# Kernel optimization log

Hardware: AMD Instinct MI355X
Metric: run time of the kernel (lower is better)

Reference implementation:

```python
import jax, jax.numpy as jnp
import numpy as np

N = 100000
C_IN, C_OUT = 128, 64
BN_EPS = 1e-5
SLOPE = 0.01  # torch LeakyReLU default


def setup_inputs() -> dict:
    key = jax.random.key(0)
    ks = jax.random.split(key, 12)

    def w(k, K, cin, cout):
        return jax.random.normal(k, (K, cin, cout), jnp.float32) / np.sqrt(K * cin)

    x_feats = jax.random.normal(ks[0], (N, C_IN), jnp.float32)
    skip_feats = jax.random.normal(ks[1], (N, C_OUT), jnp.float32)
    W1 = w(ks[2], 27, C_IN, C_OUT)
    Wt = w(ks[3], 27, C_OUT, C_OUT)
    W2 = w(ks[4], 9, C_OUT, C_OUT)
    W3 = w(ks[5], 9, C_OUT, C_OUT)
    W4 = w(ks[6], 27, C_OUT, C_OUT)
    # bn[l] = (gamma, beta, running_mean, running_var) for BN layer l
    gamma = 1.0 + 0.01 * jax.random.normal(ks[7], (4, C_OUT), jnp.float32)
    beta = 0.01 * jax.random.normal(ks[8], (4, C_OUT), jnp.float32)
    mean = 0.1 * jax.random.normal(ks[9], (4, C_OUT), jnp.float32)
    var = jax.random.uniform(ks[10], (4, C_OUT), jnp.float32, 0.5, 1.5)
    bn = jnp.stack([gamma, beta, mean, var], axis=1)  # [4, 4, C_OUT]

    nk = jax.random.split(ks[11], 5)
    nbr1 = jax.random.randint(nk[0], (27, N), 0, N, jnp.int64)
    nbrt = jax.random.randint(nk[1], (27, N), 0, N, jnp.int64)
    nbr2 = jax.random.randint(nk[2], (9, N), 0, N, jnp.int64)
    nbr3 = jax.random.randint(nk[3], (9, N), 0, N, jnp.int64)
    nbr4 = jax.random.randint(nk[4], (27, N), 0, N, jnp.int64)
    return dict(x_feats=x_feats, skip_feats=skip_feats, W1=W1, Wt=Wt, W2=W2,
                W3=W3, W4=W4, bn=bn, nbr1=nbr1, nbrt=nbrt, nbr2=nbr2,
                nbr3=nbr3, nbr4=nbr4)


def sparse_conv(feats, W, nbr):
    """Gather-GEMM-accumulate sparse conv.

    feats: [N, Cin]; W: [K, Cin, Cout]; nbr: [K, N] neighbor index per tap.
    out[i] = sum_k feats[nbr[k, i]] @ W[k]
    """
    acc0 = jnp.zeros((feats.shape[0], W.shape[-1]), feats.dtype)

    def step(acc, wn):
        w_k, idx_k = wn
        return acc + feats[idx_k] @ w_k, None

    out, _ = jax.lax.scan(step, acc0, (W, nbr))
    return out


def bn_lrelu(x, p):
    gamma, beta, mean, var = p[0], p[1], p[2], p[3]
    y = (x - mean) * jax.lax.rsqrt(var + BN_EPS) * gamma + beta
    return jnp.where(y >= 0, y, SLOPE * y)


def reference(x_feats, skip_feats, W1, Wt, W2, W3, W4, bn,
              nbr1, nbrt, nbr2, nbr3, nbr4):
    # up_block: conv3x3x3 + BN + LeakyReLU, then transposed conv (no BN/act)
    h = bn_lrelu(sparse_conv(x_feats, W1, nbr1), bn[0])
    h = sparse_conv(h, Wt, nbrt)
    h = h + skip_feats  # out.feats += skip.feats
    # conv_x3: three conv blocks
    h = bn_lrelu(sparse_conv(h, W2, nbr2), bn[1])
    h = bn_lrelu(sparse_conv(h, W3, nbr3), bn[2])
    h = bn_lrelu(sparse_conv(h, W4, nbr4), bn[3])
    return h
```

## Files before the change

### kernel.cpp

```cpp
#include <hip/hip_runtime.h>
#include <stdint.h>


typedef __bf16 bf16x8 __attribute__((ext_vector_type(8)));
typedef float f32x16 __attribute__((ext_vector_type(16)));

__device__ __forceinline__ uint16_t f2bf(float f) {
    uint32_t u = __builtin_bit_cast(uint32_t, f);
    u = (u + 0x7fffu + ((u >> 16) & 1u)) >> 16;
    return (uint16_t)u;
}

__device__ __forceinline__ bf16x8 ldb8(const uint16_t* p) {
    return __builtin_bit_cast(bf16x8, *reinterpret_cast<const uint4*>(p));
}

__global__ void convert_x(const float* __restrict__ in, uint16_t* __restrict__ out, int n8) {
    int t = blockIdx.x * blockDim.x + threadIdx.x;
    if (t >= n8) return;
    const float4* p = reinterpret_cast<const float4*>(in) + 2 * (size_t)t;
    float4 f0 = p[0], f1 = p[1];
    uint32_t w0 = (uint32_t)f2bf(f0.x) | ((uint32_t)f2bf(f0.y) << 16);
    uint32_t w1 = (uint32_t)f2bf(f0.z) | ((uint32_t)f2bf(f0.w) << 16);
    uint32_t w2 = (uint32_t)f2bf(f1.x) | ((uint32_t)f2bf(f1.y) << 16);
    uint32_t w3 = (uint32_t)f2bf(f1.z) | ((uint32_t)f2bf(f1.w) << 16);
    uint4 v; v.x = w0; v.y = w1; v.z = w2; v.w = w3;
    *reinterpret_cast<uint4*>(out + 8 * (size_t)t) = v;
}

__global__ void pack_weights(const float* __restrict__ w1, const float* __restrict__ wt,
                             const float* __restrict__ w2, const float* __restrict__ w3,
                             const float* __restrict__ w4, const float* __restrict__ bn,
                             uint16_t* __restrict__ p1, uint16_t* __restrict__ pt,
                             uint16_t* __restrict__ p2, uint16_t* __restrict__ p3,
                             uint16_t* __restrict__ p4, float* __restrict__ bnps) {
    int w = blockIdx.y;
    int t = blockIdx.x * blockDim.x + threadIdx.x;
    if (w == 5) {
        if (t < 256) {
            int l = t >> 6, c = t & 63;
            float g = bn[(l * 4 + 0) * 64 + c];
            float b = bn[(l * 4 + 1) * 64 + c];
            float m = bn[(l * 4 + 2) * 64 + c];
            float v = bn[(l * 4 + 3) * 64 + c];
            float sc = g * rsqrtf(v + 1e-5f);
            bnps[(l * 2 + 0) * 64 + c] = sc;
            bnps[(l * 2 + 1) * 64 + c] = b - m * sc;
        }
        return;
    }
    const float* src; uint16_t* dst; int K, CIN;
    switch (w) {
        case 0:  src = w1; dst = p1; K = 27; CIN = 128; break;
        case 1:  src = wt; dst = pt; K = 27; CIN = 64;  break;
        case 2:  src = w2; dst = p2; K = 9;  CIN = 64;  break;
        case 3:  src = w3; dst = p3; K = 9;  CIN = 64;  break;
        default: src = w4; dst = p4; K = 27; CIN = 64;  break;
    }
    int S = CIN / 16;
    int F = K * S * 2 * 64;
    if (t >= F) return;
    int lane = t & 63;
    int r = t >> 6;
    int nt = r & 1; r >>= 1;
    int s = r % S;
    int k = r / S;
    int c = nt * 32 + (lane & 31);
    int cib = s * 16 + (lane >> 5) * 8;
    #pragma unroll
    for (int j = 0; j < 8; ++j)
        dst[(size_t)t * 8 + j] = f2bf(src[((size_t)k * CIN + cib + j) * 64 + c]);
}

template <int CIN, int MODE>
__global__ __launch_bounds__(64)
void conv_layer(const uint16_t* __restrict__ feats,
                const uint16_t* __restrict__ wf,
                const int* __restrict__ nbr,
                const int K, const int npts,
                const float* __restrict__ bnp,
                const float* __restrict__ skip,
                uint16_t* __restrict__ outb,
                float* __restrict__ outf) {
    constexpr int S = CIN / 16;
    const int lane = threadIdx.x;
    const int l31  = lane & 31;
    const int hi   = lane >> 5;
    const int base = blockIdx.x * 64;
    const int r0 = base + l31;
    const int r1 = r0 + 32;
    const int g0 = min(r0, npts - 1);
    const int g1 = min(r1, npts - 1);

    f32x16 acc00 = {0,0,0,0,0,0,0,0,0,0,0,0,0,0,0,0};
    f32x16 acc01 = {0,0,0,0,0,0,0,0,0,0,0,0,0,0,0,0};
    f32x16 acc10 = {0,0,0,0,0,0,0,0,0,0,0,0,0,0,0,0};
    f32x16 acc11 = {0,0,0,0,0,0,0,0,0,0,0,0,0,0,0,0};

    for (int k = 0; k < K; ++k) {
        const int i0 = nbr[(size_t)k * npts + g0];
        const int i1 = nbr[(size_t)k * npts + g1];
        const uint16_t* a0p = feats + (size_t)i0 * CIN + hi * 8;
        const uint16_t* a1p = feats + (size_t)i1 * CIN + hi * 8;
        const uint16_t* bp  = wf + (size_t)k * (S * 1024) + lane * 8;
        #pragma unroll
        for (int s = 0; s < S; ++s) {
            bf16x8 a0 = ldb8(a0p + s * 16);
            bf16x8 a1 = ldb8(a1p + s * 16);
            bf16x8 b0 = ldb8(bp + s * 1024);
            bf16x8 b1 = ldb8(bp + s * 1024 + 512);
            acc00 = __builtin_amdgcn_mfma_f32_32x32x16_bf16(a0, b0, acc00, 0, 0, 0);
            acc01 = __builtin_amdgcn_mfma_f32_32x32x16_bf16(a0, b1, acc01, 0, 0, 0);
            acc10 = __builtin_amdgcn_mfma_f32_32x32x16_bf16(a1, b0, acc10, 0, 0, 0);
            acc11 = __builtin_amdgcn_mfma_f32_32x32x16_bf16(a1, b1, acc11, 0, 0, 0);
        }
    }

    const int c0 = l31, c1 = 32 + l31;
    float sc0 = 0.f, sh0 = 0.f, sc1 = 0.f, sh1 = 0.f;
    if (MODE != 1) {
        sc0 = bnp[c0]; sh0 = bnp[64 + c0];
        sc1 = bnp[c1]; sh1 = bnp[64 + c1];
    }
    #pragma unroll
    for (int reg = 0; reg < 16; ++reg) {
        const int row = (reg & 3) + 8 * (reg >> 2) + 4 * hi;
        const int gr0 = base + row;
        const int gr1 = base + 32 + row;
        float v00 = acc00[reg], v01 = acc01[reg];
        float v10 = acc10[reg], v11 = acc11[reg];
        if (MODE != 1) {
            v00 = v00 * sc0 + sh0; v00 = v00 >= 0.f ? v00 : 0.01f * v00;
            v01 = v01 * sc1 + sh1; v01 = v01 >= 0.f ? v01 : 0.01f * v01;
            v10 = v10 * sc0 + sh0; v10 = v10 >= 0.f ? v10 : 0.01f * v10;
            v11 = v11 * sc1 + sh1; v11 = v11 >= 0.f ? v11 : 0.01f * v11;
        }
        if (gr0 < npts) {
            if (MODE == 1) { v00 += skip[(size_t)gr0 * 64 + c0]; v01 += skip[(size_t)gr0 * 64 + c1]; }
            if (MODE == 2) {
                outf[(size_t)gr0 * 64 + c0] = v00; outf[(size_t)gr0 * 64 + c1] = v01;
            } else {
                outb[(size_t)gr0 * 64 + c0] = f2bf(v00); outb[(size_t)gr0 * 64 + c1] = f2bf(v01);
            }
        }
        if (gr1 < npts) {
            if (MODE == 1) { v10 += skip[(size_t)gr1 * 64 + c0]; v11 += skip[(size_t)gr1 * 64 + c1]; }
            if (MODE == 2) {
                outf[(size_t)gr1 * 64 + c0] = v10; outf[(size_t)gr1 * 64 + c1] = v11;
            } else {
                outb[(size_t)gr1 * 64 + c0] = f2bf(v10); outb[(size_t)gr1 * 64 + c1] = f2bf(v11);
            }
        }
    }
}

extern "C" void kernel_launch(void* const* d_in, const int* in_sizes, int n_in,
                              void* d_out, int out_size, void* d_ws, size_t ws_size,
                              hipStream_t stream) {
    const int N = in_sizes[0] / 128;
    const float* x    = (const float*)d_in[0];
    const float* skip = (const float*)d_in[1];
    const float* W1   = (const float*)d_in[2];
    const float* Wt   = (const float*)d_in[3];
    const float* W2   = (const float*)d_in[4];
    const float* W3   = (const float*)d_in[5];
    const float* W4   = (const float*)d_in[6];
    const float* bn   = (const float*)d_in[7];
    const int* nbr1   = (const int*)d_in[8];
    const int* nbrt   = (const int*)d_in[9];
    const int* nbr2   = (const int*)d_in[10];
    const int* nbr3   = (const int*)d_in[11];
    const int* nbr4   = (const int*)d_in[12];

    uint8_t* ws = (uint8_t*)d_ws;
    size_t off = 0;
    auto carve = [&](size_t bytes) -> void* {
        void* p = ws + off;
        off += (bytes + 255) & ~(size_t)255;
        return p;
    };
    uint16_t* xb  = (uint16_t*)carve((size_t)N * 128 * 2);
    uint16_t* hA  = (uint16_t*)carve((size_t)N * 64 * 2);
    uint16_t* hB  = (uint16_t*)carve((size_t)N * 64 * 2);
    uint16_t* p1  = (uint16_t*)carve((size_t)27 * 128 * 64 * 2);
    uint16_t* pt  = (uint16_t*)carve((size_t)27 * 64 * 64 * 2);
    uint16_t* p2  = (uint16_t*)carve((size_t)9 * 64 * 64 * 2);
    uint16_t* p3  = (uint16_t*)carve((size_t)9 * 64 * 64 * 2);
    uint16_t* p4  = (uint16_t*)carve((size_t)27 * 64 * 64 * 2);
    float*    bnp = (float*)carve((size_t)4 * 2 * 64 * 4);

    const int n8 = N * 16;
    convert_x<<<(n8 + 255) / 256, 256, 0, stream>>>(x, xb, n8);
    pack_weights<<<dim3(108, 6), 256, 0, stream>>>(W1, Wt, W2, W3, W4, bn,
                                                   p1, pt, p2, p3, p4, bnp);

    const int grid = (N + 63) / 64;
    conv_layer<128, 0><<<grid, 64, 0, stream>>>(xb, p1, nbr1, 27, N, bnp + 0,   nullptr, hA, nullptr);
    conv_layer<64,  1><<<grid, 64, 0, stream>>>(hA, pt, nbrt, 27, N, nullptr,   skip,    hB, nullptr);
    conv_layer<64,  0><<<grid, 64, 0, stream>>>(hB, p2, nbr2, 9,  N, bnp + 128, nullptr, hA, nullptr);
    conv_layer<64,  0><<<grid, 64, 0, stream>>>(hA, p3, nbr3, 9,  N, bnp + 256, nullptr, hB, nullptr);
    conv_layer<64,  2><<<grid, 64, 0, stream>>>(hB, p4, nbr4, 27, N, bnp + 384, nullptr, nullptr, (float*)d_out);
}
```

Measured before the change: 537.1 us.

## Split kernel taps across two waves with LDS reduction and prefetched gathers

Each block now covers 32 points with two waves. Each wave handles half of the kernel taps, and the two partial accumulators are summed through shared memory. For CIN=64 layers the next tap's neighbor rows are prefetched into registers while the current tap's MFMAs run. Neighbor indices use nontemporal loads, and the epilogue writes vectorized, coalesced rows instead of scattered scalar stores. This is meant to raise parallelism and memory-level latency hiding in the gather. In exchange, each B-weight fragment now feeds only one 32-row tile rather than two, and the change adds an LDS round trip and a block barrier.

```diff
diff --git a/kernel.cpp b/kernel.cpp
--- a/kernel.cpp
+++ b/kernel.cpp
@@ -72,85 +72,134 @@
         dst[(size_t)t * 8 + j] = f2bf(src[((size_t)k * CIN + cib + j) * 64 + c]);
 }
 
-template <int CIN, int MODE>
-__global__ __launch_bounds__(64)
+template <int CIN, int K, int MODE>
+__global__ __launch_bounds__(128, 4)
 void conv_layer(const uint16_t* __restrict__ feats,
                 const uint16_t* __restrict__ wf,
                 const int* __restrict__ nbr,
-                const int K, const int npts,
+                const int npts,
                 const float* __restrict__ bnp,
                 const float* __restrict__ skip,
                 uint16_t* __restrict__ outb,
                 float* __restrict__ outf) {
     constexpr int S = CIN / 16;
-    const int lane = threadIdx.x;
+    constexpr int KH = K / 2;
+    constexpr bool PREF = (CIN == 64);
+    constexpr int RS = 68;
+    __shared__ float red[2 * 32 * RS];
+
+    const int tid  = threadIdx.x;
+    const int wave = tid >> 6;
+    const int lane = tid & 63;
     const int l31  = lane & 31;
     const int hi   = lane >> 5;
-    const int base = blockIdx.x * 64;
-    const int r0 = base + l31;
-    const int r1 = r0 + 32;
-    const int g0 = min(r0, npts - 1);
-    const int g1 = min(r1, npts - 1);
-
-    f32x16 acc00 = {0,0,0,0,0,0,0,0,0,0,0,0,0,0,0,0};
-    f32x16 acc01 = {0,0,0,0,0,0,0,0,0,0,0,0,0,0,0,0};
-    f32x16 acc10 = {0,0,0,0,0,0,0,0,0,0,0,0,0,0,0,0};
-    f32x16 acc11 = {0,0,0,0,0,0,0,0,0,0,0,0,0,0,0,0};
-
-    for (int k = 0; k < K; ++k) {
-        const int i0 = nbr[(size_t)k * npts + g0];
-        const int i1 = nbr[(size_t)k * npts + g1];
-        const uint16_t* a0p = feats + (size_t)i0 * CIN + hi * 8;
-        const uint16_t* a1p = feats + (size_t)i1 * CIN + hi * 8;
-        const uint16_t* bp  = wf + (size_t)k * (S * 1024) + lane * 8;
-        #pragma unroll
-        for (int s = 0; s < S; ++s) {
-            bf16x8 a0 = ldb8(a0p + s * 16);
-            bf16x8 a1 = ldb8(a1p + s * 16);
-            bf16x8 b0 = ldb8(bp + s * 1024);
-            bf16x8 b1 = ldb8(bp + s * 1024 + 512);
-            acc00 = __builtin_amdgcn_mfma_f32_32x32x16_bf16(a0, b0, acc00, 0, 0, 0);
-            acc01 = __builtin_amdgcn_mfma_f32_32x32x16_bf16(a0, b1, acc01, 0, 0, 0);
-            acc10 = __builtin_amdgcn_mfma_f32_32x32x16_bf16(a1, b0, acc10, 0, 0, 0);
-            acc11 = __builtin_amdgcn_mfma_f32_32x32x16_bf16(a1, b1, acc11, 0, 0, 0);
-        }
-    }
-
-    const int c0 = l31, c1 = 32 + l31;
-    float sc0 = 0.f, sh0 = 0.f, sc1 = 0.f, sh1 = 0.f;
-    if (MODE != 1) {
-        sc0 = bnp[c0]; sh0 = bnp[64 + c0];
-        sc1 = bnp[c1]; sh1 = bnp[64 + c1];
-    }
+    const int base = blockIdx.x * 32;
+    const int g0   = min(base + l31, npts - 1);
+
+    const int k0  = wave ? KH : 0;
+    const int cnt = wave ? (K - KH) : KH;
+
+    const int* nb = nbr + (size_t)k0 * npts + g0;
+    const uint16_t* wb = wf + (size_t)k0 * (S * 1024) + lane * 8;
+
+    f32x16 acc0 = {0,0,0,0,0,0,0,0,0,0,0,0,0,0,0,0};
+    f32x16 acc1 = {0,0,0,0,0,0,0,0,0,0,0,0,0,0,0,0};
+
+    int ic = __builtin_nontemporal_load(nb);
+    int i1 = (cnt > 1) ? __builtin_nontemporal_load(nb + (size_t)npts) : 0;
+
+    if constexpr (PREF) {
+        bf16x8 ac[S], an[S];
+        {
+            const uint16_t* ap = feats + (size_t)ic * CIN + hi * 8;
+            #pragma unroll
+            for (int s = 0; s < S; ++s) ac[s] = ldb8(ap + s * 16);
+        }
+        for (int kk = 0; kk < cnt; ++kk) {
+            const int i2 = (kk + 2 < cnt)
+                ? __builtin_nontemporal_load(nb + (size_t)(kk + 2) * npts) : 0;
+            if (kk + 1 < cnt) {
+                const uint16_t* ap = feats + (size_t)i1 * CIN + hi * 8;
+                #pragma unroll
+                for (int s = 0; s < S; ++s) an[s] = ldb8(ap + s * 16);
+            }
+            const uint16_t* bp = wb + (size_t)kk * (S * 1024);
+            #pragma unroll
+            for (int s = 0; s < S; ++s) {
+                bf16x8 b0 = ldb8(bp + s * 1024);
+                bf16x8 b1 = ldb8(bp + s * 1024 + 512);
+                acc0 = __builtin_amdgcn_mfma_f32_32x32x16_bf16(ac[s], b0, acc0, 0, 0, 0);
+                acc1 = __builtin_amdgcn_mfma_f32_32x32x16_bf16(ac[s], b1, acc1, 0, 0, 0);
+            }
+            if (kk + 1 < cnt) {
+                #pragma unroll
+                for (int s = 0; s < S; ++s) ac[s] = an[s];
+            }
+            i1 = i2;
+        }
+    } else {
+        for (int kk = 0; kk < cnt; ++kk) {
+            const int i2 = (kk + 2 < cnt)
+                ? __builtin_nontemporal_load(nb + (size_t)(kk + 2) * npts) : 0;
+            const uint16_t* ap = feats + (size_t)ic * CIN + hi * 8;
+            bf16x8 ac[S];
+            #pragma unroll
+            for (int s = 0; s < S; ++s) ac[s] = ldb8(ap + s * 16);
+            const uint16_t* bp = wb + (size_t)kk * (S * 1024);
+            #pragma unroll
+            for (int s = 0; s < S; ++s) {
+                bf16x8 b0 = ldb8(bp + s * 1024);
+                bf16x8 b1 = ldb8(bp + s * 1024 + 512);
+                acc0 = __builtin_amdgcn_mfma_f32_32x32x16_bf16(ac[s], b0, acc0, 0, 0, 0);
+                acc1 = __builtin_amdgcn_mfma_f32_32x32x16_bf16(ac[s], b1, acc1, 0, 0, 0);
+            }
+            ic = i1; i1 = i2;
+        }
+    }
+
     #pragma unroll
     for (int reg = 0; reg < 16; ++reg) {
         const int row = (reg & 3) + 8 * (reg >> 2) + 4 * hi;
-        const int gr0 = base + row;
-        const int gr1 = base + 32 + row;
-        float v00 = acc00[reg], v01 = acc01[reg];
-        float v10 = acc10[reg], v11 = acc11[reg];
-        if (MODE != 1) {
-            v00 = v00 * sc0 + sh0; v00 = v00 >= 0.f ? v00 : 0.01f * v00;
-            v01 = v01 * sc1 + sh1; v01 = v01 >= 0.f ? v01 : 0.01f * v01;
-            v10 = v10 * sc0 + sh0; v10 = v10 >= 0.f ? v10 : 0.01f * v10;
-            v11 = v11 * sc1 + sh1; v11 = v11 >= 0.f ? v11 : 0.01f * v11;
-        }
-        if (gr0 < npts) {
-            if (MODE == 1) { v00 += skip[(size_t)gr0 * 64 + c0]; v01 += skip[(size_t)gr0 * 64 + c1]; }
-            if (MODE == 2) {
-                outf[(size_t)gr0 * 64 + c0] = v00; outf[(size_t)gr0 * 64 + c1] = v01;
-            } else {
-                outb[(size_t)gr0 * 64 + c0] = f2bf(v00); outb[(size_t)gr0 * 64 + c1] = f2bf(v01);
-            }
-        }
-        if (gr1 < npts) {
-            if (MODE == 1) { v10 += skip[(size_t)gr1 * 64 + c0]; v11 += skip[(size_t)gr1 * 64 + c1]; }
-            if (MODE == 2) {
-                outf[(size_t)gr1 * 64 + c0] = v10; outf[(size_t)gr1 * 64 + c1] = v11;
-            } else {
-                outb[(size_t)gr1 * 64 + c0] = f2bf(v10); outb[(size_t)gr1 * 64 + c1] = f2bf(v11);
-            }
-        }
+        red[wave * (32 * RS) + row * RS + l31]      = acc0[reg];
+        red[wave * (32 * RS) + row * RS + 32 + l31] = acc1[reg];
+    }
+    __syncthreads();
+
+    const int er = tid >> 2;
+    const int ec = (tid & 3) * 16;
+    const int grow = base + er;
+    if (grow >= npts) return;
+
+    float v[16];
+    #pragma unroll
+    for (int j = 0; j < 16; ++j)
+        v[j] = red[er * RS + ec + j] + red[32 * RS + er * RS + ec + j];
+
+    if constexpr (MODE == 1) {
+        const float* sp = skip + (size_t)grow * 64 + ec;
+        #pragma unroll
+        for (int j = 0; j < 16; ++j) v[j] += sp[j];
+    } else {
+        #pragma unroll
+        for (int j = 0; j < 16; ++j) {
+            float y = v[j] * bnp[ec + j] + bnp[64 + ec + j];
+            v[j] = y >= 0.f ? y : 0.01f * y;
+        }
+    }
+
+    if constexpr (MODE == 2) {
+        float4* op = reinterpret_cast<float4*>(outf + (size_t)grow * 64 + ec);
+        #pragma unroll
+        for (int q = 0; q < 4; ++q)
+            op[q] = make_float4(v[4*q+0], v[4*q+1], v[4*q+2], v[4*q+3]);
+    } else {
+        uint32_t w[8];
+        #pragma unroll
+        for (int q = 0; q < 8; ++q)
+            w[q] = (uint32_t)f2bf(v[2*q]) | ((uint32_t)f2bf(v[2*q+1]) << 16);
+        uint4* op = reinterpret_cast<uint4*>(outb + (size_t)grow * 64 + ec);
+        op[0] = make_uint4(w[0], w[1], w[2], w[3]);
+        op[1] = make_uint4(w[4], w[5], w[6], w[7]);
     }
 }
 
@@ -194,10 +243,10 @@
     pack_weights<<<dim3(108, 6), 256, 0, stream>>>(W1, Wt, W2, W3, W4, bn,
                                                    p1, pt, p2, p3, p4, bnp);
 
-    const int grid = (N + 63) / 64;
-    conv_layer<128, 0><<<grid, 64, 0, stream>>>(xb, p1, nbr1, 27, N, bnp + 0,   nullptr, hA, nullptr);
-    conv_layer<64,  1><<<grid, 64, 0, stream>>>(hA, pt, nbrt, 27, N, nullptr,   skip,    hB, nullptr);
-    conv_layer<64,  0><<<grid, 64, 0, stream>>>(hB, p2, nbr2, 9,  N, bnp + 128, nullptr, hA, nullptr);
-    conv_layer<64,  0><<<grid, 64, 0, stream>>>(hA, p3, nbr3, 9,  N, bnp + 256, nullptr, hB, nullptr);
-    conv_layer<64,  2><<<grid, 64, 0, stream>>>(hB, p4, nbr4, 27, N, bnp + 384, nullptr, nullptr, (float*)d_out);
-}
+    const int grid = (N + 31) / 32;
+    conv_layer<128, 27, 0><<<grid, 128, 0, stream>>>(xb, p1, nbr1, N, bnp + 0,   nullptr, hA, nullptr);
+    conv_layer<64,  27, 1><<<grid, 128, 0, stream>>>(hA, pt, nbrt, N, nullptr,   skip,    hB, nullptr);
+    conv_layer<64,   9, 0><<<grid, 128, 0, stream>>>(hB, p2, nbr2, N, bnp + 128, nullptr, hA, nullptr);
+    conv_layer<64,   9, 0><<<grid, 128, 0, stream>>>(hA, p3, nbr3, N, bnp + 256, nullptr, hB, nullptr);
+    conv_layer<64,  27, 2><<<grid, 128, 0, stream>>>(hB, p4, nbr4, N, bnp + 384, nullptr, nullptr, (float*)d_out);
+}
```

Result: no change. 544.6 us (+1.4%).

## Stage gathered neighbor rows through swizzled LDS with register prefetch of next tap

Applied to the files above, without the earlier changes.

Each tap's gathered feature rows are now loaded with row-contiguous vector loads, with the index broadcast by shuffle. They are held in registers, then written to an XOR-swizzled shared-memory tile, and the MFMA operands are read back from that tile. The loads for tap k+1 and the neighbor index for tap k+2 are issued before the MFMAs of tap k run, so gather latency overlaps compute. K becomes a template parameter so the loops fully specialize. This costs extra registers for the staging buffer and an LDS round-trip, and relies on single-wave ordering because there is no barrier.

```diff
diff --git a/kernel.cpp b/kernel.cpp
--- a/kernel.cpp
+++ b/kernel.cpp
@@ -72,41 +72,73 @@
         dst[(size_t)t * 8 + j] = f2bf(src[((size_t)k * CIN + cib + j) * 64 + c]);
 }
 
-template <int CIN, int MODE>
+template <int CIN, int K, int MODE>
 __global__ __launch_bounds__(64)
 void conv_layer(const uint16_t* __restrict__ feats,
                 const uint16_t* __restrict__ wf,
                 const int* __restrict__ nbr,
-                const int K, const int npts,
+                const int npts,
                 const float* __restrict__ bnp,
                 const float* __restrict__ skip,
                 uint16_t* __restrict__ outb,
                 float* __restrict__ outf) {
-    constexpr int S = CIN / 16;
+    constexpr int S    = CIN / 16;
+    constexpr int CPR  = CIN / 8;
+    constexpr int RPI  = 64 / CPR;
+    constexpr int NSTG = CPR;
+    __shared__ uint4 sm4[64 * CPR];
+
     const int lane = threadIdx.x;
     const int l31  = lane & 31;
     const int hi   = lane >> 5;
+    const int xr   = l31 & 7;
     const int base = blockIdx.x * 64;
-    const int r0 = base + l31;
-    const int r1 = r0 + 32;
-    const int g0 = min(r0, npts - 1);
-    const int g1 = min(r1, npts - 1);
+    const int g    = min(base + lane, npts - 1);
+
+    const int sub = lane >> ((CPR == 16) ? 4 : 3);
+    const int t   = lane & (CPR - 1);
+
+    const uint16_t* sm = (const uint16_t*)sm4;
 
     f32x16 acc00 = {0,0,0,0,0,0,0,0,0,0,0,0,0,0,0,0};
     f32x16 acc01 = {0,0,0,0,0,0,0,0,0,0,0,0,0,0,0,0};
     f32x16 acc10 = {0,0,0,0,0,0,0,0,0,0,0,0,0,0,0,0};
     f32x16 acc11 = {0,0,0,0,0,0,0,0,0,0,0,0,0,0,0,0};
 
-    for (int k = 0; k < K; ++k) {
-        const int i0 = nbr[(size_t)k * npts + g0];
-        const int i1 = nbr[(size_t)k * npts + g1];
-        const uint16_t* a0p = feats + (size_t)i0 * CIN + hi * 8;
-        const uint16_t* a1p = feats + (size_t)i1 * CIN + hi * 8;
-        const uint16_t* bp  = wf + (size_t)k * (S * 1024) + lane * 8;
+    uint4 st[NSTG];
+
+    {
+        const int idx0 = nbr[g];
+        #pragma unroll
+        for (int it = 0; it < NSTG; ++it) {
+            const int row = it * RPI + sub;
+            const int src = __shfl(idx0, row);
+            st[it] = *reinterpret_cast<const uint4*>(feats + (size_t)src * CIN + t * 8);
+        }
+    }
+    int idxn = (K > 1) ? nbr[(size_t)npts + g] : 0;
+
+    for (int kk = 0; kk < K; ++kk) {
+        #pragma unroll
+        for (int it = 0; it < NSTG; ++it) {
+            const int row = it * RPI + sub;
+            sm4[row * CPR + (t ^ (row & 7))] = st[it];
+        }
+        if (kk + 1 < K) {
+            #pragma unroll
+            for (int it = 0; it < NSTG; ++it) {
+                const int row = it * RPI + sub;
+                const int src = __shfl(idxn, row);
+                st[it] = *reinterpret_cast<const uint4*>(feats + (size_t)src * CIN + t * 8);
+            }
+            if (kk + 2 < K) idxn = nbr[(size_t)(kk + 2) * npts + g];
+        }
+        const uint16_t* bp = wf + (size_t)kk * (S * 1024) + lane * 8;
         #pragma unroll
         for (int s = 0; s < S; ++s) {
-            bf16x8 a0 = ldb8(a0p + s * 16);
-            bf16x8 a1 = ldb8(a1p + s * 16);
+            const int sl = (2 * s + hi) ^ xr;
+            bf16x8 a0 = ldb8(sm + (size_t)l31 * CIN + sl * 8);
+            bf16x8 a1 = ldb8(sm + (size_t)(32 + l31) * CIN + sl * 8);
             bf16x8 b0 = ldb8(bp + s * 1024);
             bf16x8 b1 = ldb8(bp + s * 1024 + 512);
             acc00 = __builtin_amdgcn_mfma_f32_32x32x16_bf16(a0, b0, acc00, 0, 0, 0);
@@ -195,9 +227,9 @@
                                                    p1, pt, p2, p3, p4, bnp);
 
     const int grid = (N + 63) / 64;
-    conv_layer<128, 0><<<grid, 64, 0, stream>>>(xb, p1, nbr1, 27, N, bnp + 0,   nullptr, hA, nullptr);
-    conv_layer<64,  1><<<grid, 64, 0, stream>>>(hA, pt, nbrt, 27, N, nullptr,   skip,    hB, nullptr);
-    conv_layer<64,  0><<<grid, 64, 0, stream>>>(hB, p2, nbr2, 9,  N, bnp + 128, nullptr, hA, nullptr);
-    conv_layer<64,  0><<<grid, 64, 0, stream>>>(hA, p3, nbr3, 9,  N, bnp + 256, nullptr, hB, nullptr);
-    conv_layer<64,  2><<<grid, 64, 0, stream>>>(hB, p4, nbr4, 27, N, bnp + 384, nullptr, nullptr, (float*)d_out);
-}
+    conv_layer<128, 27, 0><<<grid, 64, 0, stream>>>(xb, p1, nbr1, N, bnp + 0,   nullptr, hA, nullptr);
+    conv_layer<64,  27, 1><<<grid, 64, 0, stream>>>(hA, pt, nbrt, N, nullptr,   skip,    hB, nullptr);
+    conv_layer<64,   9, 0><<<grid, 64, 0, stream>>>(hB, p2, nbr2, N, bnp + 128, nullptr, hA, nullptr);
+    conv_layer<64,   9, 0><<<grid, 64, 0, stream>>>(hA, p3, nbr3, N, bnp + 256, nullptr, hB, nullptr);
+    conv_layer<64,  27, 2><<<grid, 64, 0, stream>>>(hB, p4, nbr4, N, bnp + 384, nullptr, nullptr, (float*)d_out);
+}
```

New measurement: 960.2 us. 1.79x slower.
